# Performance work log

Hardware: AMD Instinct MI355X
Metric: run time of the kernel (lower is better)

## Reference

```python
import jax, jax.numpy as jnp
import numpy as np

N_NODES = 100000
N_EDGES = 1200000
D = 64          # node_feat_size
G_FEAT = 128    # graph_feat_size
N_GRAPHS = 256
N_TASKS = 1


def setup_inputs() -> dict:
    key = jax.random.key(0)
    ks = jax.random.split(key, 12)
    node_feats = jax.random.normal(ks[0], (N_NODES, D), dtype=jnp.float32)
    edge_feats = jax.random.normal(ks[1], (N_EDGES, 8), dtype=jnp.float32)
    src = jax.random.randint(ks[2], (N_EDGES,), 0, N_NODES, dtype=jnp.int64 if jax.config.read('jax_enable_x64') else jnp.int32)
    dst = jax.random.randint(ks[3], (N_EDGES,), 0, N_NODES, dtype=src.dtype)
    graph_ids = jnp.sort(jax.random.randint(ks[4], (N_NODES,), 0, N_GRAPHS, dtype=src.dtype))
    s = 1.0 / np.sqrt(D)
    W_gcn = jax.random.uniform(ks[5], (D, D), minval=-s, maxval=s, dtype=jnp.float32)
    b_gcn = jnp.zeros((D,), jnp.float32)
    W_res = jax.random.uniform(ks[6], (D, D), minval=-s, maxval=s, dtype=jnp.float32)
    b_res = jnp.zeros((D,), jnp.float32)
    W_in = jax.random.uniform(ks[7], (D, D), minval=-s, maxval=s, dtype=jnp.float32)
    b_in = jnp.zeros((D,), jnp.float32)
    W_out = jax.random.uniform(ks[8], (D, G_FEAT), minval=-s, maxval=s, dtype=jnp.float32)
    b_out = jnp.zeros((G_FEAT,), jnp.float32)
    sp = 1.0 / np.sqrt(G_FEAT)
    W_pred = jax.random.uniform(ks[9], (G_FEAT, N_TASKS), minval=-sp, maxval=sp, dtype=jnp.float32)
    b_pred = jnp.zeros((N_TASKS,), jnp.float32)
    return dict(node_feats=node_feats, edge_feats=edge_feats, src=src, dst=dst,
                graph_ids=graph_ids, W_gcn=W_gcn, b_gcn=b_gcn, W_res=W_res, b_res=b_res,
                W_in=W_in, b_in=b_in, W_out=W_out, b_out=b_out, W_pred=W_pred, b_pred=b_pred)


def reference(node_feats, edge_feats, src, dst, graph_ids,
              W_gcn, b_gcn, W_res, b_res, W_in, b_in, W_out, b_out, W_pred, b_pred):
    # --- GCNLayer (GraphConv norm='none', activation=relu, residual=True) ---
    # message passing: copy src features, sum at dst (no normalization)
    agg = jax.ops.segment_sum(node_feats[src], dst, num_segments=N_NODES)  # [N, D]
    h = jax.nn.relu(agg @ W_gcn + b_gcn)                                   # graph_conv output
    h = h + jax.nn.relu(node_feats @ W_res + b_res)                        # residual branch
    # --- MLPNodeReadout (mode='sum') ---
    h = jax.nn.relu(h @ W_in + b_in)      # [N, D]
    h = h @ W_out + b_out                 # [N, G_FEAT]
    g_feats = jax.ops.segment_sum(h, graph_ids, num_segments=N_GRAPHS)  # [G, G_FEAT]
    # --- predict ---
    out = (g_feats @ W_pred + b_pred).reshape(-1)  # [G * n_tasks]
    return out
```

## Files before the change

### kernel.cpp

```cpp
#include <hip/hip_runtime.h>

typedef __attribute__((ext_vector_type(8))) __bf16 bf16x8;
typedef __attribute__((ext_vector_type(4))) float f32x4;

union Frag { unsigned short u[8]; bf16x8 b; };

__device__ __forceinline__ unsigned short rne_bf16(float x) {
    unsigned int u = __float_as_uint(x);
    return (unsigned short)((u + 0x7fffu + ((u >> 16) & 1u)) >> 16);
}
__device__ __forceinline__ float bf16_to_f(unsigned short h) {
    return __uint_as_float(((unsigned int)h) << 16);
}

#define MFMA16 __builtin_amdgcn_mfma_f32_16x16x32_bf16
#define SBSH 10
#define SBN 1024
#define SBCAP 13056
#define BINCHUNK 4096
#define NWFRAG (3 * 2 * 2 * 4 * 64 * 8)

__global__ __launch_bounds__(256) void prepbinA_kernel(
    const float* __restrict__ nf, const int* __restrict__ src,
    const int* __restrict__ dst,
    const float* __restrict__ Wg, const float* __restrict__ Wr,
    const float* __restrict__ Wi, const float* __restrict__ Wo,
    const float* __restrict__ bo, const float* __restrict__ Wp,
    const float* __restrict__ bp,
    unsigned short* __restrict__ nfb, unsigned short* __restrict__ wfrag,
    float* __restrict__ wfold, float* __restrict__ c0, float* __restrict__ out,
    int* __restrict__ gcursor, int* __restrict__ binned,
    int nBin, int nE, int nbS, int out_size, int nNodes) {
    __shared__ int lhist[128], lbase[128], lofs[128], lcur[128];
    __shared__ int sortedV[BINCHUNK];
    __shared__ int sortedA[BINCHUNK];
    const int t = threadIdx.x;
    if ((int)blockIdx.x < nBin) {
        const int e0 = blockIdx.x * BINCHUNK;
        const int e1 = min(e0 + BINCHUNK, nE);
        const int cnt = e1 - e0;
        for (int i = t; i < 128; i += 256) lhist[i] = 0;
        __syncthreads();
        for (int e = e0 + t; e < e1; e += 256)
            atomicAdd(&lhist[dst[e] >> SBSH], 1);
        __syncthreads();
        if (t < 128) lofs[t] = lhist[t];
        __syncthreads();
        #pragma unroll
        for (int s = 1; s < 128; s <<= 1) {
            int v = 0;
            if (t < 128 && t >= s) v = lofs[t - s];
            __syncthreads();
            if (t < 128) lofs[t] += v;
            __syncthreads();
        }
        if (t < nbS) {
            int c = lhist[t];
            lbase[t] = c ? atomicAdd(&gcursor[t], c) : 0;
            lcur[t] = lofs[t] - c;
        }
        __syncthreads();
        for (int e = e0 + t; e < e1; e += 256) {
            int d = dst[e];
            int sb = d >> SBSH;
            int p = atomicAdd(&lcur[sb], 1);
            sortedV[p] = (src[e] << SBSH) | (d & (SBN - 1));
            int r = p - (lofs[sb] - lhist[sb]);
            int gp = lbase[sb] + r;
            sortedA[p] = (gp < SBCAP) ? (sb * SBCAP + gp) : -1;
        }
        __syncthreads();
        for (int i = t; i < cnt; i += 256) {
            int ga = sortedA[i];
            if (ga >= 0) binned[ga] = sortedV[i];
        }
        return;
    }
    const int tp = ((int)blockIdx.x - nBin) * 256 + t;
    const int nth = ((int)gridDim.x - nBin) * 256;
    const float4* nf4 = (const float4*)nf;
    ushort4* nfb4 = (ushort4*)nfb;
    const int nQ = nNodes * 16;
    for (int i = tp; i < nQ; i += nth) {
        float4 v = nf4[i];
        ushort4 o;
        o.x = rne_bf16(v.x); o.y = rne_bf16(v.y);
        o.z = rne_bf16(v.z); o.w = rne_bf16(v.w);
        nfb4[i] = o;
    }
    const float* Ws[3] = {Wg, Wr, Wi};
    for (int idx = tp; idx < NWFRAG; idx += nth) {
        int j = idx & 7, lane = (idx >> 3) & 63, nt = (idx >> 9) & 3;
        int kt = (idx >> 11) & 1, part = (idx >> 12) & 1, mat = idx >> 13;
        int k = kt * 32 + ((lane >> 4) << 3) + j;
        int n = nt * 16 + (lane & 15);
        float w = Ws[mat][k * 64 + n];
        unsigned short hi = rne_bf16(w);
        wfrag[idx] = (part == 0) ? hi : rne_bf16(w - bf16_to_f(hi));
    }
    if (tp < 64) {
        float s = 0.f;
        for (int j = 0; j < 128; ++j) s += Wo[tp * 128 + j] * Wp[j];
        wfold[tp] = s;
    }
    if (tp == 0) {
        float s = 0.f;
        for (int j = 0; j < 128; ++j) s += bo[j] * Wp[j];
        c0[0] = s;
    }
    if (tp < out_size) out[tp] = bp[0];
}

__global__ __launch_bounds__(1024) void segB_kernel(
    int* __restrict__ binned, const int* __restrict__ gcursor,
    int2* __restrict__ nodeTab, int nNodes) {
    __shared__ int eL[SBCAP];
    __shared__ int deg[SBN], sc[SBN], cur[SBN];
    const int b = blockIdx.x, t = threadIdx.x;
    const int cnt = min(gcursor[b], SBCAP);
    const int bb = b * SBCAP;
    deg[t] = 0;
    __syncthreads();
    for (int i = t; i < cnt; i += 1024) {
        int p = binned[bb + i];
        eL[i] = p;
        atomicAdd(&deg[p & (SBN - 1)], 1);
    }
    __syncthreads();
    sc[t] = deg[t];
    __syncthreads();
    #pragma unroll
    for (int s = 1; s < SBN; s <<= 1) {
        int v = (t >= s) ? sc[t - s] : 0;
        __syncthreads();
        sc[t] += v;
        __syncthreads();
    }
    {
        int excl = sc[t] - deg[t];
        cur[t] = excl;
        int node = b * SBN + t;
        if (node < nNodes) nodeTab[node] = make_int2(bb + excl, deg[t]);
    }
    __syncthreads();
    for (int i = t; i < cnt; i += 1024) {
        int p = eL[i];
        int pos = atomicAdd(&cur[p & (SBN - 1)], 1);
        binned[bb + pos] = p >> SBSH;
    }
}

__global__ __launch_bounds__(256) void gather_kernel(
    const unsigned short* __restrict__ nfb, const int2* __restrict__ nodeTab,
    const int* __restrict__ srcs, unsigned short* __restrict__ aggb, int nNodes) {
    int wid = blockIdx.x * 4 + (threadIdx.x >> 6);
    if (wid >= nNodes) return;
    int lane = threadIdx.x & 63;
    int half = lane >> 5;
    int cp = lane & 31;
    int2 sd = nodeTab[wid];
    int base = sd.x, d = sd.y;
    const ushort2* nfb2 = (const ushort2*)nfb;
    float ax = 0.f, ay = 0.f;
    if (d > 0 && d <= 64) {
        int myidx = srcs[base + min(lane, d - 1)];
        int dh = (d - half + 1) >> 1;
        for (int jb = 0; jb < dh; jb += 8) {
            int sA[8];
            #pragma unroll
            for (int u = 0; u < 8; ++u) {
                int e = 2 * (jb + u) + half;
                sA[u] = __shfl(myidx, (e < d) ? e : (d - 1), 64);
            }
            ushort2 v[8];
            #pragma unroll
            for (int u = 0; u < 8; ++u)
                v[u] = nfb2[(long)sA[u] * 32 + cp];
            #pragma unroll
            for (int u = 0; u < 8; ++u)
                if (jb + u < dh) { ax += bf16_to_f(v[u].x); ay += bf16_to_f(v[u].y); }
        }
    } else if (d > 64) {
        int k = half;
        for (; k + 8 <= d; k += 8) {
            int s0 = srcs[base + k],     s1 = srcs[base + k + 2];
            int s2 = srcs[base + k + 4], s3 = srcs[base + k + 6];
            ushort2 v0 = nfb2[(long)s0 * 32 + cp];
            ushort2 v1 = nfb2[(long)s1 * 32 + cp];
            ushort2 v2 = nfb2[(long)s2 * 32 + cp];
            ushort2 v3 = nfb2[(long)s3 * 32 + cp];
            ax += (bf16_to_f(v0.x) + bf16_to_f(v1.x)) + (bf16_to_f(v2.x) + bf16_to_f(v3.x));
            ay += (bf16_to_f(v0.y) + bf16_to_f(v1.y)) + (bf16_to_f(v2.y) + bf16_to_f(v3.y));
        }
        for (; k < d; k += 2) {
            int s = srcs[base + k];
            ushort2 v = nfb2[(long)s * 32 + cp];
            ax += bf16_to_f(v.x); ay += bf16_to_f(v.y);
        }
    }
    ax += __shfl_xor(ax, 32, 64);
    ay += __shfl_xor(ay, 32, 64);
    if (half == 0) {
        ushort2 o; o.x = rne_bf16(ax); o.y = rne_bf16(ay);
        ((ushort2*)aggb)[(long)wid * 32 + cp] = o;
    }
}

__global__ __launch_bounds__(256) void mlp_kernel(
    const unsigned short* __restrict__ aggb, const unsigned short* __restrict__ nfb,
    const int* __restrict__ gids, const unsigned short* __restrict__ wfrag,
    const float* __restrict__ bg, const float* __restrict__ br,
    const float* __restrict__ bi, const float* __restrict__ wfold,
    const float* __restrict__ c0p, float* __restrict__ out, int nTiles) {
    __shared__ float hs_all[4][32 * 68];
    const int wave = threadIdx.x >> 6, lane = threadIdx.x & 63;
    const int wid = blockIdx.x * 4 + wave;
    if (wid >= nTiles) return;
    float* hs = hs_all[wave];
    const int base = wid * 32;
    const int mrow = lane & 15, quad = lane >> 4;

    Frag aA[2][2], aN[2][2];
    #pragma unroll
    for (int rt = 0; rt < 2; ++rt) {
        const unsigned short* rowA = aggb + (long)(base + rt * 16 + mrow) * 64;
        const unsigned short* rowN = nfb  + (long)(base + rt * 16 + mrow) * 64;
        #pragma unroll
        for (int kt = 0; kt < 2; ++kt) {
            aA[rt][kt].b = *(const bf16x8*)(rowA + kt * 32 + quad * 8);
            aN[rt][kt].b = *(const bf16x8*)(rowN + kt * 32 + quad * 8);
        }
    }
    const unsigned short* wl0 = wfrag + lane * 8;
    auto WF = [&](int mat, int part, int kt, int nt) -> bf16x8 {
        return *(const bf16x8*)(wl0 + (size_t)((((mat * 2 + part) * 2 + kt) * 4 + nt) * 64) * 8);
    };
    f32x4 accA[2][4], accR[2][4];
    #pragma unroll
    for (int rt = 0; rt < 2; ++rt)
        #pragma unroll
        for (int nt = 0; nt < 4; ++nt) {
            accA[rt][nt] = (f32x4){0.f, 0.f, 0.f, 0.f};
            accR[rt][nt] = (f32x4){0.f, 0.f, 0.f, 0.f};
        }
    #pragma unroll
    for (int nt = 0; nt < 4; ++nt)
        #pragma unroll
        for (int kt = 0; kt < 2; ++kt) {
            bf16x8 gh = WF(0, 0, kt, nt), gl = WF(0, 1, kt, nt);
            bf16x8 rh = WF(1, 0, kt, nt), rl = WF(1, 1, kt, nt);
            #pragma unroll
            for (int rt = 0; rt < 2; ++rt) {
                accA[rt][nt] = MFMA16(aA[rt][kt].b, gh, accA[rt][nt], 0, 0, 0);
                accA[rt][nt] = MFMA16(aA[rt][kt].b, gl, accA[rt][nt], 0, 0, 0);
                accR[rt][nt] = MFMA16(aN[rt][kt].b, rh, accR[rt][nt], 0, 0, 0);
                accR[rt][nt] = MFMA16(aN[rt][kt].b, rl, accR[rt][nt], 0, 0, 0);
            }
        }
    #pragma unroll
    for (int nt = 0; nt < 4; ++nt) {
        float bgv = bg[nt * 16 + mrow], brv = br[nt * 16 + mrow];
        #pragma unroll
        for (int rt = 0; rt < 2; ++rt)
            #pragma unroll
            for (int r = 0; r < 4; ++r) {
                float h = fmaxf(accA[rt][nt][r] + bgv, 0.f)
                        + fmaxf(accR[rt][nt][r] + brv, 0.f);
                hs[(rt * 16 + quad * 4 + r) * 68 + nt * 16 + mrow] = h;
            }
    }
    __builtin_amdgcn_wave_barrier();
    Frag aH[2][2];
    #pragma unroll
    for (int rt = 0; rt < 2; ++rt)
        #pragma unroll
        for (int kt = 0; kt < 2; ++kt) {
            const float* hp = hs + (rt * 16 + mrow) * 68 + kt * 32 + quad * 8;
            float4 v0 = *(const float4*)hp;
            float4 v1 = *(const float4*)(hp + 4);
            aH[rt][kt].u[0] = rne_bf16(v0.x); aH[rt][kt].u[1] = rne_bf16(v0.y);
            aH[rt][kt].u[2] = rne_bf16(v0.z); aH[rt][kt].u[3] = rne_bf16(v0.w);
            aH[rt][kt].u[4] = rne_bf16(v1.x); aH[rt][kt].u[5] = rne_bf16(v1.y);
            aH[rt][kt].u[6] = rne_bf16(v1.z); aH[rt][kt].u[7] = rne_bf16(v1.w);
        }
    f32x4 accH[2][4];
    #pragma unroll
    for (int rt = 0; rt < 2; ++rt)
        #pragma unroll
        for (int nt = 0; nt < 4; ++nt)
            accH[rt][nt] = (f32x4){0.f, 0.f, 0.f, 0.f};
    #pragma unroll
    for (int nt = 0; nt < 4; ++nt)
        #pragma unroll
        for (int kt = 0; kt < 2; ++kt) {
            bf16x8 ih = WF(2, 0, kt, nt), il = WF(2, 1, kt, nt);
            #pragma unroll
            for (int rt = 0; rt < 2; ++rt) {
                accH[rt][nt] = MFMA16(aH[rt][kt].b, ih, accH[rt][nt], 0, 0, 0);
                accH[rt][nt] = MFMA16(aH[rt][kt].b, il, accH[rt][nt], 0, 0, 0);
            }
        }
    float p[2][4];
    #pragma unroll
    for (int rt = 0; rt < 2; ++rt)
        #pragma unroll
        for (int r = 0; r < 4; ++r) p[rt][r] = 0.f;
    #pragma unroll
    for (int nt = 0; nt < 4; ++nt) {
        float biv = bi[nt * 16 + mrow], wfv = wfold[nt * 16 + mrow];
        #pragma unroll
        for (int rt = 0; rt < 2; ++rt)
            #pragma unroll
            for (int r = 0; r < 4; ++r)
                p[rt][r] += fmaxf(accH[rt][nt][r] + biv, 0.f) * wfv;
    }
    #pragma unroll
    for (int m = 1; m <= 8; m <<= 1)
        #pragma unroll
        for (int rt = 0; rt < 2; ++rt)
            #pragma unroll
            for (int r = 0; r < 4; ++r)
                p[rt][r] += __shfl_xor(p[rt][r], m, 64);
    const float c0 = c0p[0];
    #pragma unroll
    for (int rt = 0; rt < 2; ++rt)
        #pragma unroll
        for (int r = 0; r < 4; ++r) p[rt][r] += c0;
    int gself = gids[base + (lane & 31)];
    int g0 = __shfl(gself, 0, 64);
    if (__all(gself == g0)) {
        float pv = 0.f;
        if (mrow == 0) {
            #pragma unroll
            for (int rt = 0; rt < 2; ++rt)
                #pragma unroll
                for (int r = 0; r < 4; ++r) pv += p[rt][r];
        }
        pv += __shfl_xor(pv, 16, 64);
        pv += __shfl_xor(pv, 32, 64);
        if (lane == 0) atomicAdd(out + g0, pv);
    } else if (mrow == 0) {
        #pragma unroll
        for (int rt = 0; rt < 2; ++rt)
            #pragma unroll
            for (int r = 0; r < 4; ++r)
                atomicAdd(out + gids[base + rt * 16 + quad * 4 + r], p[rt][r]);
    }
}

extern "C" void kernel_launch(void* const* d_in, const int* in_sizes, int n_in,
                              void* d_out, int out_size, void* d_ws, size_t ws_size,
                              hipStream_t stream) {
    const float* node_feats = (const float*)d_in[0];
    const int* src  = (const int*)d_in[2];
    const int* dst  = (const int*)d_in[3];
    const int* gids = (const int*)d_in[4];
    const float* Wg = (const float*)d_in[5];
    const float* bg = (const float*)d_in[6];
    const float* Wr = (const float*)d_in[7];
    const float* br = (const float*)d_in[8];
    const float* Wi = (const float*)d_in[9];
    const float* bi = (const float*)d_in[10];
    const float* Wo = (const float*)d_in[11];
    const float* bo = (const float*)d_in[12];
    const float* Wp = (const float*)d_in[13];
    const float* bp = (const float*)d_in[14];
    float* out = (float*)d_out;

    const int nNodes = in_sizes[0] / 64;
    const int nE = in_sizes[2];
    const int nbS = (nNodes + SBN - 1) / SBN;
    const int nBin = (nE + BINCHUNK - 1) / BINCHUNK;
    const int nTiles = (nNodes + 31) / 32;

    int* gcursor = (int*)d_ws;
    int* binned  = gcursor + 128;
    int2* nodeTab = (int2*)(binned + (size_t)nbS * SBCAP);
    unsigned short* nfb  = (unsigned short*)(nodeTab + nNodes);
    unsigned short* aggb = nfb + (size_t)nNodes * 64;
    unsigned short* wfrag = aggb + (size_t)nNodes * 64;
    float* wfold = (float*)(wfrag + NWFRAG);
    float* c0 = wfold + 64;

    hipMemsetAsync(gcursor, 0, 128 * sizeof(int), stream);

    prepbinA_kernel<<<nBin + 512, 256, 0, stream>>>(
        node_feats, src, dst, Wg, Wr, Wi, Wo, bo, Wp, bp,
        nfb, wfrag, wfold, c0, out, gcursor, binned,
        nBin, nE, nbS, out_size, nNodes);

    segB_kernel<<<nbS, 1024, 0, stream>>>(binned, gcursor, nodeTab, nNodes);

    gather_kernel<<<(nNodes + 3) / 4, 256, 0, stream>>>(nfb, nodeTab, binned, aggb, nNodes);

    mlp_kernel<<<(nTiles + 3) / 4, 256, 0, stream>>>(aggb, nfb, gids, wfrag,
        bg, br, bi, wfold, c0, out, nTiles);
}
```

Baseline: 217.1 us.

## Replace edge binning and CSR gather with fp32 atomic scatter aggregation

Drops the dst-binning, per-superblock segment sort and per-node gather kernels. Each wave now processes batches of edges, reads fp32 source rows and atomically adds them into a zeroed fp32 aggregation buffer. The MLP kernel converts fp32 agg and node features to bf16 on load instead of using pre-converted bf16 copies. This removes two sorting passes and the separate bf16 conversion, but adds heavy global atomic traffic, a large memset, and doubled read bytes in the MLP.

```diff
diff --git a/kernel.cpp b/kernel.cpp
--- a/kernel.cpp
+++ b/kernel.cpp
@@ -14,89 +14,31 @@
 }
 
 #define MFMA16 __builtin_amdgcn_mfma_f32_16x16x32_bf16
-#define SBSH 10
-#define SBN 1024
-#define SBCAP 13056
-#define BINCHUNK 4096
 #define NWFRAG (3 * 2 * 2 * 4 * 64 * 8)
-
-__global__ __launch_bounds__(256) void prepbinA_kernel(
+#define EB 8
+
+__global__ __launch_bounds__(256) void prepscatter_kernel(
     const float* __restrict__ nf, const int* __restrict__ src,
     const int* __restrict__ dst,
     const float* __restrict__ Wg, const float* __restrict__ Wr,
     const float* __restrict__ Wi, const float* __restrict__ Wo,
     const float* __restrict__ bo, const float* __restrict__ Wp,
     const float* __restrict__ bp,
-    unsigned short* __restrict__ nfb, unsigned short* __restrict__ wfrag,
-    float* __restrict__ wfold, float* __restrict__ c0, float* __restrict__ out,
-    int* __restrict__ gcursor, int* __restrict__ binned,
-    int nBin, int nE, int nbS, int out_size, int nNodes) {
-    __shared__ int lhist[128], lbase[128], lofs[128], lcur[128];
-    __shared__ int sortedV[BINCHUNK];
-    __shared__ int sortedA[BINCHUNK];
+    unsigned short* __restrict__ wfrag, float* __restrict__ wfold,
+    float* __restrict__ c0, float* __restrict__ out,
+    float* __restrict__ agg, int nE, int out_size) {
     const int t = threadIdx.x;
-    if ((int)blockIdx.x < nBin) {
-        const int e0 = blockIdx.x * BINCHUNK;
-        const int e1 = min(e0 + BINCHUNK, nE);
-        const int cnt = e1 - e0;
-        for (int i = t; i < 128; i += 256) lhist[i] = 0;
-        __syncthreads();
-        for (int e = e0 + t; e < e1; e += 256)
-            atomicAdd(&lhist[dst[e] >> SBSH], 1);
-        __syncthreads();
-        if (t < 128) lofs[t] = lhist[t];
-        __syncthreads();
-        #pragma unroll
-        for (int s = 1; s < 128; s <<= 1) {
-            int v = 0;
-            if (t < 128 && t >= s) v = lofs[t - s];
-            __syncthreads();
-            if (t < 128) lofs[t] += v;
-            __syncthreads();
-        }
-        if (t < nbS) {
-            int c = lhist[t];
-            lbase[t] = c ? atomicAdd(&gcursor[t], c) : 0;
-            lcur[t] = lofs[t] - c;
-        }
-        __syncthreads();
-        for (int e = e0 + t; e < e1; e += 256) {
-            int d = dst[e];
-            int sb = d >> SBSH;
-            int p = atomicAdd(&lcur[sb], 1);
-            sortedV[p] = (src[e] << SBSH) | (d & (SBN - 1));
-            int r = p - (lofs[sb] - lhist[sb]);
-            int gp = lbase[sb] + r;
-            sortedA[p] = (gp < SBCAP) ? (sb * SBCAP + gp) : -1;
-        }
-        __syncthreads();
-        for (int i = t; i < cnt; i += 256) {
-            int ga = sortedA[i];
-            if (ga >= 0) binned[ga] = sortedV[i];
-        }
-        return;
-    }
-    const int tp = ((int)blockIdx.x - nBin) * 256 + t;
-    const int nth = ((int)gridDim.x - nBin) * 256;
-    const float4* nf4 = (const float4*)nf;
-    ushort4* nfb4 = (ushort4*)nfb;
-    const int nQ = nNodes * 16;
-    for (int i = tp; i < nQ; i += nth) {
-        float4 v = nf4[i];
-        ushort4 o;
-        o.x = rne_bf16(v.x); o.y = rne_bf16(v.y);
-        o.z = rne_bf16(v.z); o.w = rne_bf16(v.w);
-        nfb4[i] = o;
-    }
+    const int tp = (int)blockIdx.x * 256 + t;
+    const int nth = (int)gridDim.x * 256;
     const float* Ws[3] = {Wg, Wr, Wi};
     for (int idx = tp; idx < NWFRAG; idx += nth) {
-        int j = idx & 7, lane = (idx >> 3) & 63, nt = (idx >> 9) & 3;
+        int j = idx & 7, ln = (idx >> 3) & 63, nt = (idx >> 9) & 3;
         int kt = (idx >> 11) & 1, part = (idx >> 12) & 1, mat = idx >> 13;
-        int k = kt * 32 + ((lane >> 4) << 3) + j;
-        int n = nt * 16 + (lane & 15);
-        float w = Ws[mat][k * 64 + n];
-        unsigned short hi = rne_bf16(w);
-        wfrag[idx] = (part == 0) ? hi : rne_bf16(w - bf16_to_f(hi));
+        int k = kt * 32 + ((ln >> 4) << 3) + j;
+        int n = nt * 16 + (ln & 15);
+        float ww = Ws[mat][k * 64 + n];
+        unsigned short hi = rne_bf16(ww);
+        wfrag[idx] = (part == 0) ? hi : rne_bf16(ww - bf16_to_f(hi));
     }
     if (tp < 64) {
         float s = 0.f;
@@ -109,105 +51,31 @@
         c0[0] = s;
     }
     if (tp < out_size) out[tp] = bp[0];
-}
-
-__global__ __launch_bounds__(1024) void segB_kernel(
-    int* __restrict__ binned, const int* __restrict__ gcursor,
-    int2* __restrict__ nodeTab, int nNodes) {
-    __shared__ int eL[SBCAP];
-    __shared__ int deg[SBN], sc[SBN], cur[SBN];
-    const int b = blockIdx.x, t = threadIdx.x;
-    const int cnt = min(gcursor[b], SBCAP);
-    const int bb = b * SBCAP;
-    deg[t] = 0;
-    __syncthreads();
-    for (int i = t; i < cnt; i += 1024) {
-        int p = binned[bb + i];
-        eL[i] = p;
-        atomicAdd(&deg[p & (SBN - 1)], 1);
-    }
-    __syncthreads();
-    sc[t] = deg[t];
-    __syncthreads();
-    #pragma unroll
-    for (int s = 1; s < SBN; s <<= 1) {
-        int v = (t >= s) ? sc[t - s] : 0;
-        __syncthreads();
-        sc[t] += v;
-        __syncthreads();
-    }
-    {
-        int excl = sc[t] - deg[t];
-        cur[t] = excl;
-        int node = b * SBN + t;
-        if (node < nNodes) nodeTab[node] = make_int2(bb + excl, deg[t]);
-    }
-    __syncthreads();
-    for (int i = t; i < cnt; i += 1024) {
-        int p = eL[i];
-        int pos = atomicAdd(&cur[p & (SBN - 1)], 1);
-        binned[bb + pos] = p >> SBSH;
-    }
-}
-
-__global__ __launch_bounds__(256) void gather_kernel(
-    const unsigned short* __restrict__ nfb, const int2* __restrict__ nodeTab,
-    const int* __restrict__ srcs, unsigned short* __restrict__ aggb, int nNodes) {
-    int wid = blockIdx.x * 4 + (threadIdx.x >> 6);
-    if (wid >= nNodes) return;
-    int lane = threadIdx.x & 63;
-    int half = lane >> 5;
-    int cp = lane & 31;
-    int2 sd = nodeTab[wid];
-    int base = sd.x, d = sd.y;
-    const ushort2* nfb2 = (const ushort2*)nfb;
-    float ax = 0.f, ay = 0.f;
-    if (d > 0 && d <= 64) {
-        int myidx = srcs[base + min(lane, d - 1)];
-        int dh = (d - half + 1) >> 1;
-        for (int jb = 0; jb < dh; jb += 8) {
-            int sA[8];
-            #pragma unroll
-            for (int u = 0; u < 8; ++u) {
-                int e = 2 * (jb + u) + half;
-                sA[u] = __shfl(myidx, (e < d) ? e : (d - 1), 64);
-            }
-            ushort2 v[8];
-            #pragma unroll
-            for (int u = 0; u < 8; ++u)
-                v[u] = nfb2[(long)sA[u] * 32 + cp];
-            #pragma unroll
-            for (int u = 0; u < 8; ++u)
-                if (jb + u < dh) { ax += bf16_to_f(v[u].x); ay += bf16_to_f(v[u].y); }
-        }
-    } else if (d > 64) {
-        int k = half;
-        for (; k + 8 <= d; k += 8) {
-            int s0 = srcs[base + k],     s1 = srcs[base + k + 2];
-            int s2 = srcs[base + k + 4], s3 = srcs[base + k + 6];
-            ushort2 v0 = nfb2[(long)s0 * 32 + cp];
-            ushort2 v1 = nfb2[(long)s1 * 32 + cp];
-            ushort2 v2 = nfb2[(long)s2 * 32 + cp];
-            ushort2 v3 = nfb2[(long)s3 * 32 + cp];
-            ax += (bf16_to_f(v0.x) + bf16_to_f(v1.x)) + (bf16_to_f(v2.x) + bf16_to_f(v3.x));
-            ay += (bf16_to_f(v0.y) + bf16_to_f(v1.y)) + (bf16_to_f(v2.y) + bf16_to_f(v3.y));
-        }
-        for (; k < d; k += 2) {
-            int s = srcs[base + k];
-            ushort2 v = nfb2[(long)s * 32 + cp];
-            ax += bf16_to_f(v.x); ay += bf16_to_f(v.y);
-        }
-    }
-    ax += __shfl_xor(ax, 32, 64);
-    ay += __shfl_xor(ay, 32, 64);
-    if (half == 0) {
-        ushort2 o; o.x = rne_bf16(ax); o.y = rne_bf16(ay);
-        ((ushort2*)aggb)[(long)wid * 32 + cp] = o;
+    const int lane = t & 63;
+    const int gw = (int)blockIdx.x * 4 + (t >> 6);
+    const int nw = (int)gridDim.x * 4;
+    for (int e0 = gw * EB; e0 < nE; e0 += nw * EB) {
+        const int n = min(EB, nE - e0);
+        int ms = 0, md = 0;
+        if (lane < EB) {
+            int e = e0 + min(lane, n - 1);
+            ms = src[e]; md = dst[e];
+        }
+        float v[EB]; int dd[EB];
+        #pragma unroll
+        for (int u = 0; u < EB; ++u) {
+            int s = __shfl(ms, u, 64);
+            dd[u] = __shfl(md, u, 64);
+            v[u] = nf[(size_t)s * 64 + lane];
+        }
+        #pragma unroll
+        for (int u = 0; u < EB; ++u)
+            if (u < n) atomicAdd(&agg[(size_t)dd[u] * 64 + lane], v[u]);
     }
 }
 
 __global__ __launch_bounds__(256) void mlp_kernel(
-    const unsigned short* __restrict__ aggb, const unsigned short* __restrict__ nfb,
+    const float* __restrict__ agg, const float* __restrict__ nf,
     const int* __restrict__ gids, const unsigned short* __restrict__ wfrag,
     const float* __restrict__ bg, const float* __restrict__ br,
     const float* __restrict__ bi, const float* __restrict__ wfold,
@@ -223,12 +91,22 @@
     Frag aA[2][2], aN[2][2];
     #pragma unroll
     for (int rt = 0; rt < 2; ++rt) {
-        const unsigned short* rowA = aggb + (long)(base + rt * 16 + mrow) * 64;
-        const unsigned short* rowN = nfb  + (long)(base + rt * 16 + mrow) * 64;
-        #pragma unroll
-        for (int kt = 0; kt < 2; ++kt) {
-            aA[rt][kt].b = *(const bf16x8*)(rowA + kt * 32 + quad * 8);
-            aN[rt][kt].b = *(const bf16x8*)(rowN + kt * 32 + quad * 8);
+        const float* rowA = agg + (size_t)(base + rt * 16 + mrow) * 64;
+        const float* rowN = nf  + (size_t)(base + rt * 16 + mrow) * 64;
+        #pragma unroll
+        for (int kt = 0; kt < 2; ++kt) {
+            float4 a0 = *(const float4*)(rowA + kt * 32 + quad * 8);
+            float4 a1 = *(const float4*)(rowA + kt * 32 + quad * 8 + 4);
+            aA[rt][kt].u[0] = rne_bf16(a0.x); aA[rt][kt].u[1] = rne_bf16(a0.y);
+            aA[rt][kt].u[2] = rne_bf16(a0.z); aA[rt][kt].u[3] = rne_bf16(a0.w);
+            aA[rt][kt].u[4] = rne_bf16(a1.x); aA[rt][kt].u[5] = rne_bf16(a1.y);
+            aA[rt][kt].u[6] = rne_bf16(a1.z); aA[rt][kt].u[7] = rne_bf16(a1.w);
+            float4 n0 = *(const float4*)(rowN + kt * 32 + quad * 8);
+            float4 n1 = *(const float4*)(rowN + kt * 32 + quad * 8 + 4);
+            aN[rt][kt].u[0] = rne_bf16(n0.x); aN[rt][kt].u[1] = rne_bf16(n0.y);
+            aN[rt][kt].u[2] = rne_bf16(n0.z); aN[rt][kt].u[3] = rne_bf16(n0.w);
+            aN[rt][kt].u[4] = rne_bf16(n1.x); aN[rt][kt].u[5] = rne_bf16(n1.y);
+            aN[rt][kt].u[6] = rne_bf16(n1.z); aN[rt][kt].u[7] = rne_bf16(n1.w);
         }
     }
     const unsigned short* wl0 = wfrag + lane * 8;
@@ -369,30 +247,19 @@
 
     const int nNodes = in_sizes[0] / 64;
     const int nE = in_sizes[2];
-    const int nbS = (nNodes + SBN - 1) / SBN;
-    const int nBin = (nE + BINCHUNK - 1) / BINCHUNK;
     const int nTiles = (nNodes + 31) / 32;
 
-    int* gcursor = (int*)d_ws;
-    int* binned  = gcursor + 128;
-    int2* nodeTab = (int2*)(binned + (size_t)nbS * SBCAP);
-    unsigned short* nfb  = (unsigned short*)(nodeTab + nNodes);
-    unsigned short* aggb = nfb + (size_t)nNodes * 64;
-    unsigned short* wfrag = aggb + (size_t)nNodes * 64;
+    float* agg = (float*)d_ws;
+    unsigned short* wfrag = (unsigned short*)(agg + (size_t)nNodes * 64);
     float* wfold = (float*)(wfrag + NWFRAG);
     float* c0 = wfold + 64;
 
-    hipMemsetAsync(gcursor, 0, 128 * sizeof(int), stream);
-
-    prepbinA_kernel<<<nBin + 512, 256, 0, stream>>>(
+    hipMemsetAsync(agg, 0, (size_t)nNodes * 64 * sizeof(float), stream);
+
+    prepscatter_kernel<<<4096, 256, 0, stream>>>(
         node_feats, src, dst, Wg, Wr, Wi, Wo, bo, Wp, bp,
-        nfb, wfrag, wfold, c0, out, gcursor, binned,
-        nBin, nE, nbS, out_size, nNodes);
-
-    segB_kernel<<<nbS, 1024, 0, stream>>>(binned, gcursor, nodeTab, nNodes);
-
-    gather_kernel<<<(nNodes + 3) / 4, 256, 0, stream>>>(nfb, nodeTab, binned, aggb, nNodes);
-
-    mlp_kernel<<<(nTiles + 3) / 4, 256, 0, stream>>>(aggb, nfb, gids, wfrag,
-        bg, br, bi, wfold, c0, out, nTiles);
-}
+        wfrag, wfold, c0, out, agg, nE, out_size);
+
+    mlp_kernel<<<(nTiles + 3) / 4, 256, 0, stream>>>(agg, node_feats, gids,
+        wfrag, bg, br, bi, wfold, c0, out, nTiles);
+}
```

Result: slower. 395.4 us (+82.1%).
